# Optimization experiments

Measured on AMD Instinct MI355X. Metric: run time of the kernel, lower is better.

## Reference

```python
import jax, jax.numpy as jnp
import numpy as np

H = 16       # num_heads
DH = 64      # dim_head
SCALE = DH ** -0.5


def setup_inputs() -> dict:
    key = jax.random.key(0)
    k1, k2 = jax.random.split(key)
    ZT = jax.random.normal(k1, (2, 2048, 1024), dtype=jnp.float32)
    # Linear weight, shape (H*dh, dim); scaled like a typical init for stability
    W = jax.random.normal(k2, (1024, 1024), dtype=jnp.float32) * 0.02
    return {"ZT": ZT, "W": W}


def reference(ZT, W):
    b, n, dim = ZT.shape
    # UT(ZT): ZT @ W^T -> (b, n, H*dh), reshape to (b, h, n, dh)
    ZTU = jnp.einsum('bnd,ed->bne', ZT, W).reshape(b, n, H, DH).transpose(0, 2, 1, 3)
    # scores = ZTU @ ZTU^T * scale  (b, h, n, n)
    scores = jnp.einsum('bhnd,bhmd->bhnm', ZTU, ZTU) * SCALE
    attn = jax.nn.softmax(scores, axis=-1)  # dropout p=0 -> identity
    # attn @ ZTU -> (b, h, n, dh) -> (b, n, H*dh)
    ssa = jnp.einsum('bhnm,bhmd->bhnd', attn, ZTU)
    ssa = ssa.transpose(0, 2, 1, 3).reshape(b, n, H * DH)
    # UT(I).T == W (shape (H*dh, dim)); final projection back to dim
    mssa = jnp.einsum('bne,ed->bnd', ssa, W)
    # return_proj=False path: module returns (MSSA_out, MSSA_out)
    return (mssa, mssa)
```

## Files before the change

kernel.cpp:

```cpp
#include <hip/hip_runtime.h>
#include <hip/hip_bf16.h>
#include <stdint.h>

typedef __attribute__((ext_vector_type(8))) short bf16x8;
typedef __attribute__((ext_vector_type(4))) float f32x4;

#define MFMA16(a, b, c) __builtin_amdgcn_mfma_f32_16x16x32_bf16(a, b, c, 0, 0, 0)

typedef const __attribute__((address_space(1))) unsigned int* as1_u32p;
typedef __attribute__((address_space(3))) unsigned int* as3_u32p;
__device__ __forceinline__ void gl_lds16(const void* g, void* l) {
    __builtin_amdgcn_global_load_lds((as1_u32p)g, (as3_u32p)l, 16, 0, 0);
}

__device__ __forceinline__ unsigned short f2bs(float f) {
    __hip_bfloat16 h = __float2bfloat16(f);
    unsigned short s;
    __builtin_memcpy(&s, &h, 2);
    return s;
}

__device__ __forceinline__ unsigned int pk_bf16(float a, float b) {
    float2 f; f.x = a; f.y = b;
    __hip_bfloat162 h = __float22bfloat162_rn(f);
    unsigned int u;
    __builtin_memcpy(&u, &h, 4);
    return u;
}

__device__ __forceinline__ float exp2_raw(float x) {
    float r;
    asm("v_exp_f32 %0, %1" : "=v"(r) : "v"(x));
    return r;
}

#define QSCALE 0.18033688f

__global__ __launch_bounds__(256) void cvt_k(const float* __restrict__ w,
                                             const float* __restrict__ zt,
                                             unsigned short* __restrict__ wbf,
                                             unsigned short* __restrict__ wtbf,
                                             unsigned short* __restrict__ ztbf) {
    __shared__ __attribute__((aligned(16))) unsigned short T[64 * 72];
    const int tid = threadIdx.x;
    if (blockIdx.x >= 256) {
        const int i = ((int)blockIdx.x - 256) * 2048 + tid * 8;
        const float4 v0 = *(const float4*)(zt + i);
        const float4 v1 = *(const float4*)(zt + i + 4);
        uint4 wv;
        wv.x = pk_bf16(v0.x, v0.y);
        wv.y = pk_bf16(v0.z, v0.w);
        wv.z = pk_bf16(v1.x, v1.y);
        wv.w = pk_bf16(v1.z, v1.w);
        *(uint4*)(ztbf + i) = wv;
        return;
    }
    const int b2 = blockIdx.x;
    const int e0 = (b2 >> 4) * 64, d0 = (b2 & 15) * 64;
    const int el = tid >> 2;
    const int dl = (tid & 3) * 16;
    const float* src = w + (size_t)(e0 + el) * 1024 + d0 + dl;
    unsigned short myv[16];
#pragma unroll
    for (int q = 0; q < 4; ++q) {
        const float4 v = *(const float4*)(src + q * 4);
        myv[q * 4 + 0] = f2bs(v.x);
        myv[q * 4 + 1] = f2bs(v.y);
        myv[q * 4 + 2] = f2bs(v.z);
        myv[q * 4 + 3] = f2bs(v.w);
    }
    *(bf16x8*)(wbf + (size_t)(e0 + el) * 1024 + d0 + dl) = *(const bf16x8*)&myv[0];
    *(bf16x8*)(wbf + (size_t)(e0 + el) * 1024 + d0 + dl + 8) = *(const bf16x8*)&myv[8];
#pragma unroll
    for (int q = 0; q < 16; ++q) T[(dl + q) * 72 + el] = myv[q];
    __syncthreads();
#pragma unroll
    for (int p = 0; p < 2; ++p) {
        const int idx = p * 256 + tid;
        const int dd = idx >> 3, c = (idx & 7) * 8;
        const bf16x8 v = *(const bf16x8*)&T[dd * 72 + c];
        *(bf16x8*)(wtbf + (size_t)(d0 + dd) * 1024 + e0 + c) = v;
    }
}

template <int EPI>
__global__ __launch_bounds__(256, 2) void gemm_bt_k(
    const __hip_bfloat16* __restrict__ Abf, const __hip_bfloat16* __restrict__ B,
    unsigned short* __restrict__ ztu, unsigned short* __restrict__ ztut,
    float* __restrict__ out0, float* __restrict__ out1) {
    __shared__ __attribute__((aligned(16))) unsigned short smem[24576];
    unsigned short* Tb = smem;

    const int p = blockIdx.x;
    const int bm = (p & 7) * 8 + ((p >> 3) & 7);
    const int bn = p >> 6;
    const int tid = threadIdx.x;
    const int wave = tid >> 6, lane = tid & 63;
    const int wm = wave >> 1, wn = wave & 1;
    const int quad = lane >> 4, l16 = lane & 15;

    f32x4 acc[2][4] = {};

    const int lrow = lane >> 3;
    const int sw = (lane & 7) ^ lrow;
    const __hip_bfloat16* Ag0 = Abf + (size_t)(bm * 64 + (2 * wave) * 8 + lrow) * 1024 + sw * 8;
    const __hip_bfloat16* Ag1 = Ag0 + 8 * 1024;
    const __hip_bfloat16* Bg0 = B + (size_t)(bn * 128 + (4 * wave) * 8 + lrow) * 1024 + sw * 8;
    const __hip_bfloat16* Bg1 = Bg0 + 8 * 1024;
    const __hip_bfloat16* Bg2 = Bg0 + 16 * 1024;
    const __hip_bfloat16* Bg3 = Bg0 + 24 * 1024;

    auto stage = [&](int ko, unsigned short* sb) {
        gl_lds16(Ag0 + ko, sb + (2 * wave) * 512);
        gl_lds16(Ag1 + ko, sb + (2 * wave + 1) * 512);
        gl_lds16(Bg0 + ko, sb + 4096 + (4 * wave) * 512);
        gl_lds16(Bg1 + ko, sb + 4096 + (4 * wave + 1) * 512);
        gl_lds16(Bg2 + ko, sb + 4096 + (4 * wave + 2) * 512);
        gl_lds16(Bg3 + ko, sb + 4096 + (4 * wave + 3) * 512);
    };

    const int ch0 = (quad ^ (l16 & 7)) * 8;
    const int ch1 = ch0 ^ 32;
    const int raA = (wm * 32 + l16) * 64;
    const int raB = (wn * 64 + l16) * 64;

    stage(0, smem);
    __syncthreads();

    for (int kt = 0; kt < 16; ++kt) {
        unsigned short* const sb = smem + (kt & 1) * 12288;
        if (kt < 15) stage((kt + 1) << 6, smem + (((kt & 1) ^ 1) * 12288));
        bf16x8 af[2][2], bfr[2][4];
#pragma unroll
        for (int i = 0; i < 2; ++i) {
            af[0][i] = *(const bf16x8*)&sb[raA + i * 1024 + ch0];
            af[1][i] = *(const bf16x8*)&sb[raA + i * 1024 + ch1];
        }
#pragma unroll
        for (int j = 0; j < 4; ++j) {
            bfr[0][j] = *(const bf16x8*)&sb[4096 + raB + j * 1024 + ch0];
            bfr[1][j] = *(const bf16x8*)&sb[4096 + raB + j * 1024 + ch1];
        }
#pragma unroll
        for (int h = 0; h < 2; ++h)
#pragma unroll
            for (int i = 0; i < 2; ++i)
#pragma unroll
                for (int j = 0; j < 4; ++j) acc[i][j] = MFMA16(af[h][i], bfr[h][j], acc[i][j]);
        __syncthreads();
    }

    if (EPI == 0) {
        const int h = bn * 2 + wn;
        const int bb = bm >> 5;
        const int nb = (bm & 31) * 64;
        const size_t hb = (size_t)(bb * 16 + h) * 131072;
#pragma unroll
        for (int i = 0; i < 2; ++i) {
#pragma unroll
            for (int r = 0; r < 4; ++r) {
                const int n = nb + wm * 32 + i * 16 + quad * 4 + r;
                uint2 pk;
                pk.x = pk_bf16(acc[i][0][r], acc[i][1][r]);
                pk.y = pk_bf16(acc[i][2][r], acc[i][3][r]);
                *(uint2*)(ztu + hb + n * 64 + l16 * 4) = pk;
                const int npl = wm * 32 + quad * 8 + i * 4 + r;
                Tb[(wn * 64 + 0 + l16) * 72 + npl] = (unsigned short)(pk.x & 0xffff);
                Tb[(wn * 64 + 16 + l16) * 72 + npl] = (unsigned short)(pk.x >> 16);
                Tb[(wn * 64 + 32 + l16) * 72 + npl] = (unsigned short)(pk.y & 0xffff);
                Tb[(wn * 64 + 48 + l16) * 72 + npl] = (unsigned short)(pk.y >> 16);
            }
        }
        __syncthreads();
#pragma unroll
        for (int ee = 0; ee < 4; ++ee) {
            const int e_local = wave * 32 + ee * 8 + (lane >> 3);
            const int nc = (lane & 7) * 8;
            const bf16x8 v = *(const bf16x8*)&Tb[e_local * 72 + nc];
            const int hh = bn * 2 + (e_local >> 6);
            const int dh = e_local & 63;
            *(bf16x8*)(ztut + (size_t)(bb * 16 + hh) * 131072 + dh * 2048 + nb + nc) = v;
        }
    } else {
#pragma unroll
        for (int i = 0; i < 2; ++i) {
#pragma unroll
            for (int r = 0; r < 4; ++r) {
                const int mm = bm * 64 + wm * 32 + i * 16 + quad * 4 + r;
#pragma unroll
                for (int j = 0; j < 4; ++j) {
                    const int e = bn * 128 + wn * 64 + j * 16 + l16;
                    const float v = acc[i][j][r];
                    out0[(size_t)mm * 1024 + e] = v;
                    out1[(size_t)mm * 1024 + e] = v;
                }
            }
        }
    }
}

__global__ __launch_bounds__(256, 2) void attn_k(const unsigned short* __restrict__ ztu,
                                                 const unsigned short* __restrict__ ztut,
                                                 unsigned short* __restrict__ ssa) {
    __shared__ __attribute__((aligned(16))) unsigned short Kt[64 * 64];
    __shared__ __attribute__((aligned(16))) unsigned short Vt[64 * 64];
    const int p = blockIdx.x;
    const int ii = p >> 3;
    const int bh = (p & 7) * 4 + (ii >> 4);
    const int qt = ii & 15;
    const int tid = threadIdx.x, wave = tid >> 6, lane = tid & 63;
    const int quad = lane >> 4, l16 = lane & 15;
    const unsigned short* base = ztu + (size_t)bh * 131072;
    const unsigned short* baseT = ztut + (size_t)bh * 131072;

    const int qb = qt * 128 + wave * 32;
    bf16x8 qa[2][2];
#pragma unroll
    for (int g = 0; g < 2; ++g) {
        qa[g][0] = *(const bf16x8*)(base + (qb + g * 16 + l16) * 64 + quad * 8);
        qa[g][1] = *(const bf16x8*)(base + (qb + g * 16 + l16) * 64 + 32 + quad * 8);
    }

    float lsum[2] = {0.f, 0.f};
    f32x4 o[2][4] = {};

    const int c0 = wave * 2, c1 = c0 + 1;
    const int lrow = lane >> 3;
    const int sw = (lane & 7) ^ lrow;
    const unsigned short* gK0 = base + (c0 * 8 + lrow) * 64 + sw * 8;
    const unsigned short* gK1 = base + (c1 * 8 + lrow) * 64 + sw * 8;
    const unsigned short* gV0 = baseT + (size_t)(c0 * 8 + lrow) * 2048 + sw * 8;
    const unsigned short* gV1 = baseT + (size_t)(c1 * 8 + lrow) * 2048 + sw * 8;
    unsigned short* lK0 = &Kt[c0 * 512];
    unsigned short* lK1 = &Kt[c1 * 512];
    unsigned short* lV0 = &Vt[c0 * 512];
    unsigned short* lV1 = &Vt[c1 * 512];

    const int swq = (quad ^ (l16 & 7));
    const int koff0 = l16 * 64 + swq * 8;
    const int koff1 = l16 * 64 + (swq ^ 4) * 8;

    for (int t = 0; t < 32; ++t) {
        gl_lds16(gK0 + t * 4096, lK0);
        gl_lds16(gK1 + t * 4096, lK1);
        gl_lds16(gV0 + t * 64, lV0);
        gl_lds16(gV1 + t * 64, lV1);
        __syncthreads();

        f32x4 st[2][4];
#pragma unroll
        for (int nf = 0; nf < 4; ++nf) {
            bf16x8 kb0 = *(const bf16x8*)&Kt[nf * 1024 + koff0];
            bf16x8 kb1 = *(const bf16x8*)&Kt[nf * 1024 + koff1];
#pragma unroll
            for (int g = 0; g < 2; ++g) {
                f32x4 z = {0.f, 0.f, 0.f, 0.f};
                z = MFMA16(kb0, qa[g][0], z);
                z = MFMA16(kb1, qa[g][1], z);
                st[g][nf] = z;
            }
        }

        bf16x8 pa[2][2];
#pragma unroll
        for (int g = 0; g < 2; ++g) {
            float e[16];
#pragma unroll
            for (int nf = 0; nf < 4; ++nf)
#pragma unroll
                for (int r = 0; r < 4; ++r) e[nf * 4 + r] = exp2_raw(st[g][nf][r] * QSCALE);
            float s0 = 0.f, s1 = 0.f;
#pragma unroll
            for (int q = 0; q < 8; ++q) { s0 += e[q]; s1 += e[q + 8]; }
            lsum[g] += s0 + s1;
            uint4 u0, u1;
            u0.x = pk_bf16(e[0], e[1]);   u0.y = pk_bf16(e[2], e[3]);
            u0.z = pk_bf16(e[4], e[5]);   u0.w = pk_bf16(e[6], e[7]);
            u1.x = pk_bf16(e[8], e[9]);   u1.y = pk_bf16(e[10], e[11]);
            u1.z = pk_bf16(e[12], e[13]); u1.w = pk_bf16(e[14], e[15]);
            __builtin_memcpy(&pa[g][0], &u0, 16);
            __builtin_memcpy(&pa[g][1], &u1, 16);
        }

#pragma unroll
        for (int df = 0; df < 4; ++df) {
            bf16x8 vb0 = *(const bf16x8*)&Vt[df * 1024 + koff0];
            bf16x8 vb1 = *(const bf16x8*)&Vt[df * 1024 + koff1];
#pragma unroll
            for (int g = 0; g < 2; ++g) {
                o[g][df] = MFMA16(vb0, pa[g][0], o[g][df]);
                o[g][df] = MFMA16(vb1, pa[g][1], o[g][df]);
            }
        }
        __syncthreads();
    }

    const int b = bh >> 4, h = bh & 15;
#pragma unroll
    for (int g = 0; g < 2; ++g) {
        float v = lsum[g];
        v += __shfl_xor(v, 16);
        v += __shfl_xor(v, 32);
        const float inv = 1.0f / v;
        const int token = b * 2048 + qb + g * 16 + l16;
#pragma unroll
        for (int df = 0; df < 4; ++df) {
            uint2 pk;
            pk.x = pk_bf16(o[g][df][0] * inv, o[g][df][1] * inv);
            pk.y = pk_bf16(o[g][df][2] * inv, o[g][df][3] * inv);
            *(uint2*)(ssa + (size_t)token * 1024 + h * 64 + df * 16 + quad * 4) = pk;
        }
    }
}

extern "C" void kernel_launch(void* const* d_in, const int* in_sizes, int n_in,
                              void* d_out, int out_size, void* d_ws, size_t ws_size,
                              hipStream_t stream) {
    const float* ZT = (const float*)d_in[0];
    const float* W = (const float*)d_in[1];
    float* out = (float*)d_out;
    char* ws = (char*)d_ws;

    unsigned short* wbf   = (unsigned short*)(ws);
    unsigned short* wtbf  = (unsigned short*)(ws + 2u * 1024 * 1024);
    unsigned short* ztu   = (unsigned short*)(ws + 4u * 1024 * 1024);
    unsigned short* ztut  = (unsigned short*)(ws + 12u * 1024 * 1024);
    unsigned short* scr20 = (unsigned short*)(ws + 20u * 1024 * 1024);

    cvt_k<<<2304, 256, 0, stream>>>(W, ZT, wbf, wtbf, scr20);
    gemm_bt_k<0><<<512, 256, 0, stream>>>((const __hip_bfloat16*)scr20,
                                          (const __hip_bfloat16*)wbf, ztu, ztut,
                                          nullptr, nullptr);
    attn_k<<<512, 256, 0, stream>>>(ztu, ztut, scr20);
    gemm_bt_k<1><<<512, 256, 0, stream>>>((const __hip_bfloat16*)scr20,
                                          (const __hip_bfloat16*)wtbf, nullptr, nullptr,
                                          out, out + 4194304);
}
```

Before: 154.4 us.

## Halve attention query tile per block and compute row sums via MFMA

Each wave now handles 16 query rows instead of 32, so blocks cover 64 rows and the attention grid doubles to 1024 blocks. Softmax row sums are accumulated with an MFMA against a ones vector instead of scalar adds and cross-lane shuffles. This aims to raise occupancy and parallelism and to cut VALU work, at the cost of loading each K/V tile twice as often overall and reducing MFMA reuse of LDS fragments.

```diff
diff --git a/kernel.cpp b/kernel.cpp
--- a/kernel.cpp
+++ b/kernel.cpp
@@ -206,23 +206,23 @@
     __shared__ __attribute__((aligned(16))) unsigned short Vt[64 * 64];
     const int p = blockIdx.x;
     const int ii = p >> 3;
-    const int bh = (p & 7) * 4 + (ii >> 4);
-    const int qt = ii & 15;
+    const int bh = (p & 7) * 4 + (ii >> 5);
+    const int qt = ii & 31;
     const int tid = threadIdx.x, wave = tid >> 6, lane = tid & 63;
     const int quad = lane >> 4, l16 = lane & 15;
     const unsigned short* base = ztu + (size_t)bh * 131072;
     const unsigned short* baseT = ztut + (size_t)bh * 131072;
 
-    const int qb = qt * 128 + wave * 32;
-    bf16x8 qa[2][2];
-#pragma unroll
-    for (int g = 0; g < 2; ++g) {
-        qa[g][0] = *(const bf16x8*)(base + (qb + g * 16 + l16) * 64 + quad * 8);
-        qa[g][1] = *(const bf16x8*)(base + (qb + g * 16 + l16) * 64 + 32 + quad * 8);
-    }
-
-    float lsum[2] = {0.f, 0.f};
-    f32x4 o[2][4] = {};
+    const int qrow = qt * 64 + wave * 16;
+    bf16x8 qa[2];
+    qa[0] = *(const bf16x8*)(base + (qrow + l16) * 64 + quad * 8);
+    qa[1] = *(const bf16x8*)(base + (qrow + l16) * 64 + 32 + quad * 8);
+
+    f32x4 o[4] = {};
+    f32x4 lacc = {};
+    bf16x8 ones;
+#pragma unroll
+    for (int z = 0; z < 8; ++z) ones[z] = (short)0x3f80;
 
     const int c0 = wave * 2, c1 = c0 + 1;
     const int lrow = lane >> 3;
@@ -247,69 +247,52 @@
         gl_lds16(gV1 + t * 64, lV1);
         __syncthreads();
 
-        f32x4 st[2][4];
+        f32x4 st[4];
 #pragma unroll
         for (int nf = 0; nf < 4; ++nf) {
-            bf16x8 kb0 = *(const bf16x8*)&Kt[nf * 1024 + koff0];
-            bf16x8 kb1 = *(const bf16x8*)&Kt[nf * 1024 + koff1];
-#pragma unroll
-            for (int g = 0; g < 2; ++g) {
-                f32x4 z = {0.f, 0.f, 0.f, 0.f};
-                z = MFMA16(kb0, qa[g][0], z);
-                z = MFMA16(kb1, qa[g][1], z);
-                st[g][nf] = z;
-            }
-        }
-
-        bf16x8 pa[2][2];
-#pragma unroll
-        for (int g = 0; g < 2; ++g) {
-            float e[16];
-#pragma unroll
-            for (int nf = 0; nf < 4; ++nf)
-#pragma unroll
-                for (int r = 0; r < 4; ++r) e[nf * 4 + r] = exp2_raw(st[g][nf][r] * QSCALE);
-            float s0 = 0.f, s1 = 0.f;
-#pragma unroll
-            for (int q = 0; q < 8; ++q) { s0 += e[q]; s1 += e[q + 8]; }
-            lsum[g] += s0 + s1;
-            uint4 u0, u1;
-            u0.x = pk_bf16(e[0], e[1]);   u0.y = pk_bf16(e[2], e[3]);
-            u0.z = pk_bf16(e[4], e[5]);   u0.w = pk_bf16(e[6], e[7]);
-            u1.x = pk_bf16(e[8], e[9]);   u1.y = pk_bf16(e[10], e[11]);
-            u1.z = pk_bf16(e[12], e[13]); u1.w = pk_bf16(e[14], e[15]);
-            __builtin_memcpy(&pa[g][0], &u0, 16);
-            __builtin_memcpy(&pa[g][1], &u1, 16);
-        }
+            const bf16x8 kb0 = *(const bf16x8*)&Kt[nf * 1024 + koff0];
+            const bf16x8 kb1 = *(const bf16x8*)&Kt[nf * 1024 + koff1];
+            f32x4 z = {0.f, 0.f, 0.f, 0.f};
+            z = MFMA16(kb0, qa[0], z);
+            z = MFMA16(kb1, qa[1], z);
+            st[nf] = z;
+        }
+
+        float e[16];
+#pragma unroll
+        for (int nf = 0; nf < 4; ++nf)
+#pragma unroll
+            for (int r = 0; r < 4; ++r) e[nf * 4 + r] = exp2_raw(st[nf][r] * QSCALE);
+        bf16x8 pa[2];
+        uint4 u0, u1;
+        u0.x = pk_bf16(e[0], e[1]);   u0.y = pk_bf16(e[2], e[3]);
+        u0.z = pk_bf16(e[4], e[5]);   u0.w = pk_bf16(e[6], e[7]);
+        u1.x = pk_bf16(e[8], e[9]);   u1.y = pk_bf16(e[10], e[11]);
+        u1.z = pk_bf16(e[12], e[13]); u1.w = pk_bf16(e[14], e[15]);
+        __builtin_memcpy(&pa[0], &u0, 16);
+        __builtin_memcpy(&pa[1], &u1, 16);
+        lacc = MFMA16(ones, pa[0], lacc);
+        lacc = MFMA16(ones, pa[1], lacc);
 
 #pragma unroll
         for (int df = 0; df < 4; ++df) {
-            bf16x8 vb0 = *(const bf16x8*)&Vt[df * 1024 + koff0];
-            bf16x8 vb1 = *(const bf16x8*)&Vt[df * 1024 + koff1];
-#pragma unroll
-            for (int g = 0; g < 2; ++g) {
-                o[g][df] = MFMA16(vb0, pa[g][0], o[g][df]);
-                o[g][df] = MFMA16(vb1, pa[g][1], o[g][df]);
-            }
+            const bf16x8 vb0 = *(const bf16x8*)&Vt[df * 1024 + koff0];
+            const bf16x8 vb1 = *(const bf16x8*)&Vt[df * 1024 + koff1];
+            o[df] = MFMA16(vb0, pa[0], o[df]);
+            o[df] = MFMA16(vb1, pa[1], o[df]);
         }
         __syncthreads();
     }
 
     const int b = bh >> 4, h = bh & 15;
-#pragma unroll
-    for (int g = 0; g < 2; ++g) {
-        float v = lsum[g];
-        v += __shfl_xor(v, 16);
-        v += __shfl_xor(v, 32);
-        const float inv = 1.0f / v;
-        const int token = b * 2048 + qb + g * 16 + l16;
-#pragma unroll
-        for (int df = 0; df < 4; ++df) {
-            uint2 pk;
-            pk.x = pk_bf16(o[g][df][0] * inv, o[g][df][1] * inv);
-            pk.y = pk_bf16(o[g][df][2] * inv, o[g][df][3] * inv);
-            *(uint2*)(ssa + (size_t)token * 1024 + h * 64 + df * 16 + quad * 4) = pk;
-        }
+    const float inv = 1.0f / lacc[0];
+    const int token = b * 2048 + qrow + l16;
+#pragma unroll
+    for (int df = 0; df < 4; ++df) {
+        uint2 pk;
+        pk.x = pk_bf16(o[df][0] * inv, o[df][1] * inv);
+        pk.y = pk_bf16(o[df][2] * inv, o[df][3] * inv);
+        *(uint2*)(ssa + (size_t)token * 1024 + h * 64 + df * 16 + quad * 4) = pk;
     }
 }
 
@@ -331,7 +314,7 @@
     gemm_bt_k<0><<<512, 256, 0, stream>>>((const __hip_bfloat16*)scr20,
                                           (const __hip_bfloat16*)wbf, ztu, ztut,
                                           nullptr, nullptr);
-    attn_k<<<512, 256, 0, stream>>>(ztu, ztut, scr20);
+    attn_k<<<1024, 256, 0, stream>>>(ztu, ztut, scr20);
     gemm_bt_k<1><<<512, 256, 0, stream>>>((const __hip_bfloat16*)scr20,
                                           (const __hip_bfloat16*)wtbf, nullptr, nullptr,
                                           out, out + 4194304);
```

Result: no change. 152.2 us (-1.4%).
